# Kernel tuning notes

Measured on AMD Instinct MI355X. Metric: run time of the kernel, lower is better.

## Reference

```python
import jax, jax.numpy as jnp
import numpy as np

N_NODES = 1024
FEAT = 64
NEG_BIG = -9e15

def setup_inputs() -> dict:
    key = jax.random.key(0)
    ks = jax.random.split(key, 12)
    B, S, D = 4, 16384, FEAT
    flow_features = jax.random.normal(ks[0], (B, S, D), dtype=jnp.float32)
    src_ips = jax.random.randint(ks[1], (B, S), 0, N_NODES)
    dst_ips = jax.random.randint(ks[2], (B, S), 0, N_NODES)
    flow_volumes = jax.random.uniform(ks[3], (B, S), dtype=jnp.float32) * 2000.0
    emb = jax.random.normal(ks[4], (N_NODES, D), dtype=jnp.float32) * 0.02
    We1 = jax.random.normal(ks[5], (2 * D, 32), dtype=jnp.float32) * 0.1
    be1 = jnp.zeros((32,), dtype=jnp.float32)
    We2 = jax.random.normal(ks[6], (32, 1), dtype=jnp.float32) * 0.1
    be2 = jnp.zeros((1,), dtype=jnp.float32)
    W = jax.random.normal(ks[7], (D, D), dtype=jnp.float32) * 0.1
    a1 = jax.random.normal(ks[8], (D,), dtype=jnp.float32) * 0.1
    a2 = jax.random.normal(ks[9], (D,), dtype=jnp.float32) * 0.1
    return dict(flow_features=flow_features, src_ips=src_ips, dst_ips=dst_ips,
                flow_volumes=flow_volumes, emb=emb, We1=We1, be1=be1, We2=We2,
                be2=be2, W=W, a1=a1, a2=a2)

def _forward(flow_features, flow_volumes, emb, We1, be1, We2, be2, W, a1, a2,
             src_ips, dst_ips):
    B, S, D = flow_features.shape
    N = emb.shape[0]
    # --- DynamicGraphBuilder: scatter-add flow features at dst nodes ---
    node = jax.vmap(lambda f, d: jnp.zeros((N, D), f.dtype).at[d].add(f))(
        flow_features, dst_ips)                         # (B, N, D)
    nrm = jnp.maximum(jnp.linalg.norm(node, axis=-1, keepdims=True), 1e-12)
    h = node / nrm                                      # F.normalize(p=2)
    # --- edge weights: MLP over concat(src_emb, dst_emb), scaled by volume ---
    pair = jnp.concatenate([emb[src_ips], emb[dst_ips]], axis=-1)  # (B, S, 2D)
    mid = jax.nn.relu(pair @ We1 + be1)
    ew = jax.nn.sigmoid((mid @ We2 + be2)[..., 0])      # (B, S)
    w = ew * jax.nn.sigmoid(flow_volumes / 1000.0)
    adj = jax.vmap(lambda s, d, ww: jnp.zeros((N, N), ww.dtype)
                   .at[s, d].set(ww).at[d, s].set(ww))(src_ips, dst_ips, w)
    # --- GraphAttentionLayer (decomposed e_ij = a1.Wh_i + a2.Wh_j) ---
    Wh = h @ W                                          # (B, N, D)
    f1 = Wh @ a1                                        # (B, N)
    f2 = Wh @ a2                                        # (B, N)
    e = jax.nn.leaky_relu(f1[:, :, None] + f2[:, None, :], 0.2)  # (B, N, N)
    attn = jax.nn.softmax(jnp.where(adj > 0, e, NEG_BIG), axis=-1)
    return jax.nn.elu(jnp.einsum('bij,bjd->bid', attn, Wh))       # (B, N, D)

def reference(flow_features, src_ips, dst_ips, flow_volumes, emb, We1, be1,
              We2, be2, W, a1, a2):
    return _forward(flow_features, flow_volumes, emb, We1, be1, We2, be2,
                    W, a1, a2, src_ips, dst_ips)
```

## Files before the change

### kernel.cpp

```cpp
#include <hip/hip_runtime.h>
#include <math.h>

#define BB 4
#define SS 16384
#define NN 1024
#define DD 64
#define MW 32
#define CAP 256
#define JCAP 256

__device__ __forceinline__ float wave_sum(float v) {
    #pragma unroll
    for (int off = 32; off > 0; off >>= 1) v += __shfl_xor(v, off, 64);
    return v;
}
__device__ __forceinline__ float wave_max(float v) {
    #pragma unroll
    for (int off = 32; off > 0; off >>= 1) v = fmaxf(v, __shfl_xor(v, off, 64));
    return v;
}

__global__ __launch_bounds__(256) void build_kernel(
        const int* __restrict__ src_ips, const int* __restrict__ dst_ips,
        int* __restrict__ count, int* __restrict__ bucket,
        unsigned int* __restrict__ mask) {
    int tid = blockIdx.x * 256 + threadIdx.x;
    int b   = tid >> 14;
    int dst = dst_ips[tid];
    int src = src_ips[tid];
    int row = (b << 10) + dst;
    int pos = atomicAdd(count + row, 1);
    if (pos < CAP) bucket[row * CAP + pos] = tid;
    unsigned int* mb = mask + (size_t)b * NN * MW;
    atomicOr(mb + src * MW + (dst >> 5), 1u << (dst & 31));
    atomicOr(mb + dst * MW + (src >> 5), 1u << (src & 31));
}

__global__ __launch_bounds__(256) void gather_transform_kernel(
        const float* __restrict__ ff, const int* __restrict__ count,
        const int* __restrict__ bucket, const float* __restrict__ W,
        const float* __restrict__ a1, const float* __restrict__ a2,
        float* __restrict__ Wh, float* __restrict__ f1, float* __restrict__ f2) {
    __shared__ float Ws[DD * DD];
    __shared__ float hs[4][DD];
    __shared__ float a1s[DD], a2s[DD];
    int t = threadIdx.x;
    for (int i = t; i < DD * DD / 4; i += 256)
        ((float4*)Ws)[i] = ((const float4*)W)[i];
    if (t < DD) { a1s[t] = a1[t]; a2s[t] = a2[t]; }
    int wave = t >> 6, lane = t & 63;
    int fq = lane >> 4;
    int qi = lane & 15;
    int row = blockIdx.x * 4 + wave;

    int cnt = min(count[row], CAP);
    const int* bk = bucket + (size_t)row * CAP;
    int bkreg = (lane < cnt) ? bk[lane] : 0;
    float4 v = make_float4(0.f, 0.f, 0.f, 0.f);
    int lim = min(cnt, 64);
    for (int base = 0; base < lim; base += 4) {
        int fi = base + fq;
        int flow = __shfl(bkreg, fi, 64);
        if (fi < lim) {
            float4 x = ((const float4*)(ff + (size_t)flow * DD))[qi];
            v.x += x.x; v.y += x.y; v.z += x.z; v.w += x.w;
        }
    }
    for (int base = 64; base < cnt; base += 4) {
        int fi = base + fq;
        if (fi < cnt) {
            int flow = bk[fi];
            float4 x = ((const float4*)(ff + (size_t)flow * DD))[qi];
            v.x += x.x; v.y += x.y; v.z += x.z; v.w += x.w;
        }
    }
    #pragma unroll
    for (int off = 16; off <= 32; off <<= 1) {
        v.x += __shfl_xor(v.x, off, 64);
        v.y += __shfl_xor(v.y, off, 64);
        v.z += __shfl_xor(v.z, off, 64);
        v.w += __shfl_xor(v.w, off, 64);
    }
    float ssq = (fq == 0) ? (v.x*v.x + v.y*v.y + v.z*v.z + v.w*v.w) : 0.f;
    float nrm = fmaxf(sqrtf(wave_sum(ssq)), 1e-12f);
    float inv = 1.f / nrm;
    __syncthreads();
    if (fq == 0)
        ((float4*)hs[wave])[qi] = make_float4(v.x*inv, v.y*inv, v.z*inv, v.w*inv);
    float whl = 0.f;
    #pragma unroll
    for (int k = 0; k < DD; ++k)
        whl = fmaf(hs[wave][k], Ws[k * DD + lane], whl);
    Wh[row * DD + lane] = whl;
    float p1 = wave_sum(whl * a1s[lane]);
    float p2 = wave_sum(whl * a2s[lane]);
    if (lane == 0) { f1[row] = p1; f2[row] = p2; }
}

__global__ __launch_bounds__(256) void attn_kernel(
        const unsigned int* __restrict__ mask, const float* __restrict__ f1,
        const float* __restrict__ f2, const float* __restrict__ Wh,
        float* __restrict__ out) {
    __shared__ int   jls[4][JCAP];
    __shared__ float pls[4][JCAP];
    int t = threadIdx.x;
    int wave = t >> 6, lane = t & 63;
    int row = blockIdx.x * 4 + wave;
    int b = row >> 10;
    unsigned int mword = (lane < MW) ? mask[(size_t)row * MW + lane] : 0u;
    const float* f2b = f2 + b * NN;
    const float* Whb = Wh + (size_t)(b << 10) * DD;
    float f1i = f1[row];

    int pc = __popc(mword);
    int x = pc;
    #pragma unroll
    for (int off = 1; off < 64; off <<= 1) {
        int y = __shfl_up(x, off, 64);
        if (lane >= off) x += y;
    }
    int cnt = __shfl(x, 63, 64);
    int o = x - pc;
    if (cnt <= JCAP) {
        unsigned int bits = mword;
        while (bits) {
            int bidx = __ffs(bits) - 1; bits &= bits - 1;
            jls[wave][o++] = (lane << 5) + bidx;
        }
    }

    int fq = lane >> 4;
    int qi = lane & 15;

    if (cnt > 0 && cnt <= JCAP) {
        float m = -INFINITY;
        for (int k = lane; k < cnt; k += 64) {
            int j = jls[wave][k];
            float e = f1i + f2b[j];
            e = (e >= 0.f) ? e : 0.2f * e;
            m = fmaxf(m, e);
        }
        m = wave_max(m);
        float lsum = 0.f;
        for (int k = lane; k < cnt; k += 64) {
            int j = jls[wave][k];
            float e = f1i + f2b[j];
            e = (e >= 0.f) ? e : 0.2f * e;
            float p = __expf(e - m);
            pls[wave][k] = p;
            lsum += p;
        }
        lsum = wave_sum(lsum);
        float4 acc = make_float4(0.f, 0.f, 0.f, 0.f);
        for (int k = fq; k < cnt; k += 4) {
            int j   = jls[wave][k];
            float p = pls[wave][k];
            float4 w = ((const float4*)(Whb + (size_t)j * DD))[qi];
            acc.x = fmaf(p, w.x, acc.x);
            acc.y = fmaf(p, w.y, acc.y);
            acc.z = fmaf(p, w.z, acc.z);
            acc.w = fmaf(p, w.w, acc.w);
        }
        #pragma unroll
        for (int off = 16; off <= 32; off <<= 1) {
            acc.x += __shfl_xor(acc.x, off, 64);
            acc.y += __shfl_xor(acc.y, off, 64);
            acc.z += __shfl_xor(acc.z, off, 64);
            acc.w += __shfl_xor(acc.w, off, 64);
        }
        if (fq == 0) {
            float inv = 1.f / lsum;
            float4 r;
            r.x = acc.x * inv; r.y = acc.y * inv;
            r.z = acc.z * inv; r.w = acc.w * inv;
            r.x = (r.x > 0.f) ? r.x : expm1f(r.x);
            r.y = (r.y > 0.f) ? r.y : expm1f(r.y);
            r.z = (r.z > 0.f) ? r.z : expm1f(r.z);
            r.w = (r.w > 0.f) ? r.w : expm1f(r.w);
            ((float4*)(out + (size_t)row * DD))[qi] = r;
        }
    } else if (cnt == 0) {
        float4 acc = make_float4(0.f, 0.f, 0.f, 0.f);
        for (int k = fq; k < NN; k += 4) {
            float4 w = ((const float4*)(Whb + (size_t)k * DD))[qi];
            acc.x += w.x; acc.y += w.y; acc.z += w.z; acc.w += w.w;
        }
        #pragma unroll
        for (int off = 16; off <= 32; off <<= 1) {
            acc.x += __shfl_xor(acc.x, off, 64);
            acc.y += __shfl_xor(acc.y, off, 64);
            acc.z += __shfl_xor(acc.z, off, 64);
            acc.w += __shfl_xor(acc.w, off, 64);
        }
        if (fq == 0) {
            float4 r;
            r.x = acc.x * (1.f / NN); r.y = acc.y * (1.f / NN);
            r.z = acc.z * (1.f / NN); r.w = acc.w * (1.f / NN);
            r.x = (r.x > 0.f) ? r.x : expm1f(r.x);
            r.y = (r.y > 0.f) ? r.y : expm1f(r.y);
            r.z = (r.z > 0.f) ? r.z : expm1f(r.z);
            r.w = (r.w > 0.f) ? r.w : expm1f(r.w);
            ((float4*)(out + (size_t)row * DD))[qi] = r;
        }
    } else {
        float m = -INFINITY;
        for (int tt = 0; tt < 16; ++tt) {
            int j = lane + (tt << 6);
            unsigned int wv = __shfl(mword, j >> 5, 64);
            if (wv & (1u << (j & 31))) {
                float e = f1i + f2b[j];
                e = (e >= 0.f) ? e : 0.2f * e;
                m = fmaxf(m, e);
            }
        }
        m = wave_max(m);
        float lsum = 0.f;
        for (int tt = 0; tt < 16; ++tt) {
            int j = lane + (tt << 6);
            unsigned int wv = __shfl(mword, j >> 5, 64);
            if (wv & (1u << (j & 31))) {
                float e = f1i + f2b[j];
                e = (e >= 0.f) ? e : 0.2f * e;
                lsum += __expf(e - m);
            }
        }
        lsum = wave_sum(lsum);
        float acc = 0.f;
        for (int w = 0; w < MW; ++w) {
            unsigned int bits = __shfl(mword, w, 64);
            while (bits) {
                int j = (w << 5) + (__ffs(bits) - 1);
                bits &= bits - 1;
                float e = f1i + f2b[j];
                e = (e >= 0.f) ? e : 0.2f * e;
                acc = fmaf(__expf(e - m), Whb[(size_t)j * DD + lane], acc);
            }
        }
        acc /= lsum;
        out[(size_t)row * DD + lane] = (acc > 0.f) ? acc : expm1f(acc);
    }
}

extern "C" void kernel_launch(void* const* d_in, const int* in_sizes, int n_in,
                              void* d_out, int out_size, void* d_ws, size_t ws_size,
                              hipStream_t stream) {
    const float* ff      = (const float*)d_in[0];
    const int*   src_ips = (const int*)d_in[1];
    const int*   dst_ips = (const int*)d_in[2];
    const float* W  = (const float*)d_in[9];
    const float* a1 = (const float*)d_in[10];
    const float* a2 = (const float*)d_in[11];
    float* out = (float*)d_out;

    char* ws = (char*)d_ws;
    int* count         = (int*)ws;
    unsigned int* mask = (unsigned int*)(ws + (16 << 10));
    float* f1          = (float*)(ws + (528 << 10));
    float* f2          = (float*)(ws + (544 << 10));
    int* bucket        = (int*)(ws + (1 << 20));
    float* Wh          = (float*)(ws + (5 << 20));

    hipMemsetAsync(count, 0, (528 << 10), stream);

    build_kernel<<<BB * SS / 256, 256, 0, stream>>>(src_ips, dst_ips, count, bucket, mask);
    gather_transform_kernel<<<BB * NN / 4, 256, 0, stream>>>(ff, count, bucket, W, a1, a2, Wh, f1, f2);
    attn_kernel<<<BB * NN / 4, 256, 0, stream>>>(mask, f1, f2, Wh, out);
}
```

Baseline: 108.2 us.

## Replace global adjacency bitmask with per-node src/dst buckets built in shared memory

The build kernel no longer sets a 512KB global bitmask with atomicOr. It now records dst-side buckets, with the src node packed into the high bits, and src-side buckets holding the dst node. The attention kernel rebuilds each row's neighbor bitmask in shared memory from these two buckets, which also shrinks the memset. JCAP is raised so the dense fallback path can be dropped, and both the gather loop and the attention aggregation loop get two-way accumulator unrolling for more memory-level parallelism. The cost is a second bucket array and the extra per-row bucket reads in the attention kernel.

Result: faster. 103.6 us (-4.2%).

```diff
diff --git a/kernel.cpp b/kernel.cpp
--- a/kernel.cpp
+++ b/kernel.cpp
@@ -7,7 +7,7 @@
 #define DD 64
 #define MW 32
 #define CAP 256
-#define JCAP 256
+#define JCAP 512
 
 __device__ __forceinline__ float wave_sum(float v) {
     #pragma unroll
@@ -22,23 +22,23 @@
 
 __global__ __launch_bounds__(256) void build_kernel(
         const int* __restrict__ src_ips, const int* __restrict__ dst_ips,
-        int* __restrict__ count, int* __restrict__ bucket,
-        unsigned int* __restrict__ mask) {
+        int* __restrict__ cntd, int* __restrict__ cnts,
+        int* __restrict__ bucket_d, int* __restrict__ bucket_s) {
     int tid = blockIdx.x * 256 + threadIdx.x;
     int b   = tid >> 14;
     int dst = dst_ips[tid];
     int src = src_ips[tid];
-    int row = (b << 10) + dst;
-    int pos = atomicAdd(count + row, 1);
-    if (pos < CAP) bucket[row * CAP + pos] = tid;
-    unsigned int* mb = mask + (size_t)b * NN * MW;
-    atomicOr(mb + src * MW + (dst >> 5), 1u << (dst & 31));
-    atomicOr(mb + dst * MW + (src >> 5), 1u << (src & 31));
+    int rd = (b << 10) + dst;
+    int rs = (b << 10) + src;
+    int pd = atomicAdd(cntd + rd, 1);
+    if (pd < CAP) bucket_d[rd * CAP + pd] = tid | (src << 16);
+    int ps = atomicAdd(cnts + rs, 1);
+    if (ps < CAP) bucket_s[rs * CAP + ps] = dst;
 }
 
 __global__ __launch_bounds__(256) void gather_transform_kernel(
-        const float* __restrict__ ff, const int* __restrict__ count,
-        const int* __restrict__ bucket, const float* __restrict__ W,
+        const float* __restrict__ ff, const int* __restrict__ cntd,
+        const int* __restrict__ bucket_d, const float* __restrict__ W,
         const float* __restrict__ a1, const float* __restrict__ a2,
         float* __restrict__ Wh, float* __restrict__ f1, float* __restrict__ f2) {
     __shared__ float Ws[DD * DD];
@@ -53,27 +53,35 @@
     int qi = lane & 15;
     int row = blockIdx.x * 4 + wave;
 
-    int cnt = min(count[row], CAP);
-    const int* bk = bucket + (size_t)row * CAP;
+    int cnt = min(cntd[row], CAP);
+    const int* bk = bucket_d + (size_t)row * CAP;
     int bkreg = (lane < cnt) ? bk[lane] : 0;
-    float4 v = make_float4(0.f, 0.f, 0.f, 0.f);
+    float4 v0 = make_float4(0.f, 0.f, 0.f, 0.f);
+    float4 v1 = make_float4(0.f, 0.f, 0.f, 0.f);
     int lim = min(cnt, 64);
-    for (int base = 0; base < lim; base += 4) {
-        int fi = base + fq;
-        int flow = __shfl(bkreg, fi, 64);
-        if (fi < lim) {
-            float4 x = ((const float4*)(ff + (size_t)flow * DD))[qi];
-            v.x += x.x; v.y += x.y; v.z += x.z; v.w += x.w;
+    for (int base = 0; base < lim; base += 8) {
+        int fi0 = base + fq;
+        int fi1 = base + 4 + fq;
+        int w0 = __shfl(bkreg, fi0, 64);
+        int w1 = __shfl(bkreg, fi1, 64);
+        if (fi0 < lim) {
+            float4 x = ((const float4*)(ff + (size_t)(w0 & 0xFFFF) * DD))[qi];
+            v0.x += x.x; v0.y += x.y; v0.z += x.z; v0.w += x.w;
+        }
+        if (fi1 < lim) {
+            float4 x = ((const float4*)(ff + (size_t)(w1 & 0xFFFF) * DD))[qi];
+            v1.x += x.x; v1.y += x.y; v1.z += x.z; v1.w += x.w;
         }
     }
     for (int base = 64; base < cnt; base += 4) {
         int fi = base + fq;
         if (fi < cnt) {
-            int flow = bk[fi];
+            int flow = bk[fi] & 0xFFFF;
             float4 x = ((const float4*)(ff + (size_t)flow * DD))[qi];
-            v.x += x.x; v.y += x.y; v.z += x.z; v.w += x.w;
-        }
-    }
+            v0.x += x.x; v0.y += x.y; v0.z += x.z; v0.w += x.w;
+        }
+    }
+    float4 v = make_float4(v0.x + v1.x, v0.y + v1.y, v0.z + v1.z, v0.w + v1.w);
     #pragma unroll
     for (int off = 16; off <= 32; off <<= 1) {
         v.x += __shfl_xor(v.x, off, 64);
@@ -98,16 +106,31 @@
 }
 
 __global__ __launch_bounds__(256) void attn_kernel(
-        const unsigned int* __restrict__ mask, const float* __restrict__ f1,
-        const float* __restrict__ f2, const float* __restrict__ Wh,
-        float* __restrict__ out) {
+        const int* __restrict__ cntd, const int* __restrict__ cnts,
+        const int* __restrict__ bucket_d, const int* __restrict__ bucket_s,
+        const float* __restrict__ f1, const float* __restrict__ f2,
+        const float* __restrict__ Wh, float* __restrict__ out) {
+    __shared__ unsigned int bms[4][MW];
     __shared__ int   jls[4][JCAP];
     __shared__ float pls[4][JCAP];
     int t = threadIdx.x;
     int wave = t >> 6, lane = t & 63;
     int row = blockIdx.x * 4 + wave;
     int b = row >> 10;
-    unsigned int mword = (lane < MW) ? mask[(size_t)row * MW + lane] : 0u;
+    if (lane < MW) bms[wave][lane] = 0u;
+    int c1 = min(cntd[row], CAP);
+    int c2 = min(cnts[row], CAP);
+    const int* bd = bucket_d + (size_t)row * CAP;
+    const int* bs = bucket_s + (size_t)row * CAP;
+    for (int k = lane; k < c1; k += 64) {
+        int cand = (bd[k] >> 16) & 0x3FF;
+        atomicOr(&bms[wave][cand >> 5], 1u << (cand & 31));
+    }
+    for (int k = lane; k < c2; k += 64) {
+        int cand = bs[k] & 0x3FF;
+        atomicOr(&bms[wave][cand >> 5], 1u << (cand & 31));
+    }
+    unsigned int mword = (lane < MW) ? bms[wave][lane] : 0u;
     const float* f2b = f2 + b * NN;
     const float* Whb = Wh + (size_t)(b << 10) * DD;
     float f1i = f1[row];
@@ -121,7 +144,7 @@
     }
     int cnt = __shfl(x, 63, 64);
     int o = x - pc;
-    if (cnt <= JCAP) {
+    {
         unsigned int bits = mword;
         while (bits) {
             int bidx = __ffs(bits) - 1; bits &= bits - 1;
@@ -132,7 +155,7 @@
     int fq = lane >> 4;
     int qi = lane & 15;
 
-    if (cnt > 0 && cnt <= JCAP) {
+    if (cnt > 0) {
         float m = -INFINITY;
         for (int k = lane; k < cnt; k += 64) {
             int j = jls[wave][k];
@@ -151,16 +174,29 @@
             lsum += p;
         }
         lsum = wave_sum(lsum);
-        float4 acc = make_float4(0.f, 0.f, 0.f, 0.f);
-        for (int k = fq; k < cnt; k += 4) {
-            int j   = jls[wave][k];
-            float p = pls[wave][k];
-            float4 w = ((const float4*)(Whb + (size_t)j * DD))[qi];
-            acc.x = fmaf(p, w.x, acc.x);
-            acc.y = fmaf(p, w.y, acc.y);
-            acc.z = fmaf(p, w.z, acc.z);
-            acc.w = fmaf(p, w.w, acc.w);
-        }
+        float4 a0 = make_float4(0.f, 0.f, 0.f, 0.f);
+        float4 a1 = make_float4(0.f, 0.f, 0.f, 0.f);
+        for (int k = fq; k < cnt; k += 8) {
+            int j0   = jls[wave][k];
+            float p0 = pls[wave][k];
+            float4 w0 = ((const float4*)(Whb + (size_t)j0 * DD))[qi];
+            a0.x = fmaf(p0, w0.x, a0.x);
+            a0.y = fmaf(p0, w0.y, a0.y);
+            a0.z = fmaf(p0, w0.z, a0.z);
+            a0.w = fmaf(p0, w0.w, a0.w);
+            int k1 = k + 4;
+            if (k1 < cnt) {
+                int j1   = jls[wave][k1];
+                float p1 = pls[wave][k1];
+                float4 w1 = ((const float4*)(Whb + (size_t)j1 * DD))[qi];
+                a1.x = fmaf(p1, w1.x, a1.x);
+                a1.y = fmaf(p1, w1.y, a1.y);
+                a1.z = fmaf(p1, w1.z, a1.z);
+                a1.w = fmaf(p1, w1.w, a1.w);
+            }
+        }
+        float4 acc = make_float4(a0.x + a1.x, a0.y + a1.y,
+                                 a0.z + a1.z, a0.w + a1.w);
         #pragma unroll
         for (int off = 16; off <= 32; off <<= 1) {
             acc.x += __shfl_xor(acc.x, off, 64);
@@ -179,7 +215,7 @@
             r.w = (r.w > 0.f) ? r.w : expm1f(r.w);
             ((float4*)(out + (size_t)row * DD))[qi] = r;
         }
-    } else if (cnt == 0) {
+    } else {
         float4 acc = make_float4(0.f, 0.f, 0.f, 0.f);
         for (int k = fq; k < NN; k += 4) {
             float4 w = ((const float4*)(Whb + (size_t)k * DD))[qi];
@@ -202,42 +238,6 @@
             r.w = (r.w > 0.f) ? r.w : expm1f(r.w);
             ((float4*)(out + (size_t)row * DD))[qi] = r;
         }
-    } else {
-        float m = -INFINITY;
-        for (int tt = 0; tt < 16; ++tt) {
-            int j = lane + (tt << 6);
-            unsigned int wv = __shfl(mword, j >> 5, 64);
-            if (wv & (1u << (j & 31))) {
-                float e = f1i + f2b[j];
-                e = (e >= 0.f) ? e : 0.2f * e;
-                m = fmaxf(m, e);
-            }
-        }
-        m = wave_max(m);
-        float lsum = 0.f;
-        for (int tt = 0; tt < 16; ++tt) {
-            int j = lane + (tt << 6);
-            unsigned int wv = __shfl(mword, j >> 5, 64);
-            if (wv & (1u << (j & 31))) {
-                float e = f1i + f2b[j];
-                e = (e >= 0.f) ? e : 0.2f * e;
-                lsum += __expf(e - m);
-            }
-        }
-        lsum = wave_sum(lsum);
-        float acc = 0.f;
-        for (int w = 0; w < MW; ++w) {
-            unsigned int bits = __shfl(mword, w, 64);
-            while (bits) {
-                int j = (w << 5) + (__ffs(bits) - 1);
-                bits &= bits - 1;
-                float e = f1i + f2b[j];
-                e = (e >= 0.f) ? e : 0.2f * e;
-                acc = fmaf(__expf(e - m), Whb[(size_t)j * DD + lane], acc);
-            }
-        }
-        acc /= lsum;
-        out[(size_t)row * DD + lane] = (acc > 0.f) ? acc : expm1f(acc);
     }
 }
 
@@ -253,16 +253,20 @@
     float* out = (float*)d_out;
 
     char* ws = (char*)d_ws;
-    int* count         = (int*)ws;
-    unsigned int* mask = (unsigned int*)(ws + (16 << 10));
-    float* f1          = (float*)(ws + (528 << 10));
-    float* f2          = (float*)(ws + (544 << 10));
-    int* bucket        = (int*)(ws + (1 << 20));
-    float* Wh          = (float*)(ws + (5 << 20));
-
-    hipMemsetAsync(count, 0, (528 << 10), stream);
-
-    build_kernel<<<BB * SS / 256, 256, 0, stream>>>(src_ips, dst_ips, count, bucket, mask);
-    gather_transform_kernel<<<BB * NN / 4, 256, 0, stream>>>(ff, count, bucket, W, a1, a2, Wh, f1, f2);
-    attn_kernel<<<BB * NN / 4, 256, 0, stream>>>(mask, f1, f2, Wh, out);
-}
+    int* cntd       = (int*)ws;
+    int* cnts       = (int*)(ws + (16 << 10));
+    float* f1       = (float*)(ws + (32 << 10));
+    float* f2       = (float*)(ws + (48 << 10));
+    int* bucket_d   = (int*)(ws + (1 << 20));
+    int* bucket_s   = (int*)(ws + (5 << 20));
+    float* Wh       = (float*)(ws + (9 << 20));
+
+    hipMemsetAsync(cntd, 0, (32 << 10), stream);
+
+    build_kernel<<<BB * SS / 256, 256, 0, stream>>>(src_ips, dst_ips,
+                                                    cntd, cnts, bucket_d, bucket_s);
+    gather_transform_kernel<<<BB * NN / 4, 256, 0, stream>>>(ff, cntd, bucket_d,
+                                                             W, a1, a2, Wh, f1, f2);
+    attn_kernel<<<BB * NN / 4, 256, 0, stream>>>(cntd, cnts, bucket_d, bucket_s,
+                                                 f1, f2, Wh, out);
+}
```

## Replace global-atomic graph build with per-block index scans in shared memory

Applied to the files above, without the earlier changes.

Removes the memset and the global-atomic build kernel. Each block now scans the batch's whole dst (and src) index arrays to build its own per-row flow lists and adjacency bitmasks in shared memory, and each block handles 8 rows instead of 4. This trades global atomics, the extra launch and the bucket/mask global traffic for redundant reading of the index arrays: each block reads 64KB to 128KB of indices, with 512 blocks per kernel. The gather and accumulate loops are also unrolled by two. The per-row flow list is capped at 192 entries, and rows past that cap are silently truncated.

Result: slower. 110.7 us (+2.3%).

```diff
diff --git a/kernel.cpp b/kernel.cpp
--- a/kernel.cpp
+++ b/kernel.cpp
@@ -6,7 +6,8 @@
 #define NN 1024
 #define DD 64
 #define MW 32
-#define CAP 256
+#define RPB 8
+#define FCAP 192
 #define JCAP 256
 
 __device__ __forceinline__ float wave_sum(float v) {
@@ -20,224 +21,264 @@
     return v;
 }
 
-__global__ __launch_bounds__(256) void build_kernel(
-        const int* __restrict__ src_ips, const int* __restrict__ dst_ips,
-        int* __restrict__ count, int* __restrict__ bucket,
-        unsigned int* __restrict__ mask) {
-    int tid = blockIdx.x * 256 + threadIdx.x;
-    int b   = tid >> 14;
-    int dst = dst_ips[tid];
-    int src = src_ips[tid];
-    int row = (b << 10) + dst;
-    int pos = atomicAdd(count + row, 1);
-    if (pos < CAP) bucket[row * CAP + pos] = tid;
-    unsigned int* mb = mask + (size_t)b * NN * MW;
-    atomicOr(mb + src * MW + (dst >> 5), 1u << (dst & 31));
-    atomicOr(mb + dst * MW + (src >> 5), 1u << (src & 31));
-}
-
-__global__ __launch_bounds__(256) void gather_transform_kernel(
-        const float* __restrict__ ff, const int* __restrict__ count,
-        const int* __restrict__ bucket, const float* __restrict__ W,
-        const float* __restrict__ a1, const float* __restrict__ a2,
-        float* __restrict__ Wh, float* __restrict__ f1, float* __restrict__ f2) {
+__global__ __launch_bounds__(256) void gather_transform_scan(
+        const float* __restrict__ ff, const int* __restrict__ dst_ips,
+        const float* __restrict__ W, const float* __restrict__ a1,
+        const float* __restrict__ a2, float* __restrict__ Wh,
+        float* __restrict__ f1, float* __restrict__ f2) {
     __shared__ float Ws[DD * DD];
+    __shared__ float a1s[DD], a2s[DD];
     __shared__ float hs[4][DD];
-    __shared__ float a1s[DD], a2s[DD];
+    __shared__ int lcnt[RPB];
+    __shared__ int lst[RPB][FCAP];
     int t = threadIdx.x;
     for (int i = t; i < DD * DD / 4; i += 256)
         ((float4*)Ws)[i] = ((const float4*)W)[i];
     if (t < DD) { a1s[t] = a1[t]; a2s[t] = a2[t]; }
+    if (t < RPB) lcnt[t] = 0;
+    __syncthreads();
+
+    int blk = blockIdx.x;
+    int b = blk >> 7;
+    int n0 = (blk & 127) * RPB;
+    const int* db = dst_ips + b * SS;
+
+    for (int f4 = t; f4 < SS / 4; f4 += 256) {
+        int4 d = ((const int4*)db)[f4];
+        int f = f4 << 2;
+        #define CHK(c, off) { unsigned r = (unsigned)(c - n0); \
+            if (r < RPB) { int p = atomicAdd(&lcnt[r], 1); \
+                           if (p < FCAP) lst[r][p] = f + off; } }
+        CHK(d.x, 0) CHK(d.y, 1) CHK(d.z, 2) CHK(d.w, 3)
+        #undef CHK
+    }
+    __syncthreads();
+
     int wave = t >> 6, lane = t & 63;
     int fq = lane >> 4;
     int qi = lane & 15;
-    int row = blockIdx.x * 4 + wave;
-
-    int cnt = min(count[row], CAP);
-    const int* bk = bucket + (size_t)row * CAP;
-    int bkreg = (lane < cnt) ? bk[lane] : 0;
-    float4 v = make_float4(0.f, 0.f, 0.f, 0.f);
-    int lim = min(cnt, 64);
-    for (int base = 0; base < lim; base += 4) {
-        int fi = base + fq;
-        int flow = __shfl(bkreg, fi, 64);
-        if (fi < lim) {
-            float4 x = ((const float4*)(ff + (size_t)flow * DD))[qi];
-            v.x += x.x; v.y += x.y; v.z += x.z; v.w += x.w;
-        }
+    const float* ffb = ff + (size_t)b * SS * DD;
+
+    for (int rr = 0; rr < 2; ++rr) {
+        int lr = wave * 2 + rr;
+        int row = blk * RPB + lr;
+        int cnt = min(lcnt[lr], FCAP);
+        float4 v0 = make_float4(0.f, 0.f, 0.f, 0.f);
+        float4 v1 = make_float4(0.f, 0.f, 0.f, 0.f);
+        for (int k = fq; k < cnt; k += 8) {
+            int F0 = lst[lr][k];
+            float4 x = ((const float4*)(ffb + (size_t)F0 * DD))[qi];
+            v0.x += x.x; v0.y += x.y; v0.z += x.z; v0.w += x.w;
+            int k1 = k + 4;
+            if (k1 < cnt) {
+                int F1 = lst[lr][k1];
+                float4 y = ((const float4*)(ffb + (size_t)F1 * DD))[qi];
+                v1.x += y.x; v1.y += y.y; v1.z += y.z; v1.w += y.w;
+            }
+        }
+        float4 v = make_float4(v0.x + v1.x, v0.y + v1.y,
+                               v0.z + v1.z, v0.w + v1.w);
+        #pragma unroll
+        for (int off = 16; off <= 32; off <<= 1) {
+            v.x += __shfl_xor(v.x, off, 64);
+            v.y += __shfl_xor(v.y, off, 64);
+            v.z += __shfl_xor(v.z, off, 64);
+            v.w += __shfl_xor(v.w, off, 64);
+        }
+        float ssq = (fq == 0) ? (v.x*v.x + v.y*v.y + v.z*v.z + v.w*v.w) : 0.f;
+        float nrm = fmaxf(sqrtf(wave_sum(ssq)), 1e-12f);
+        float inv = 1.f / nrm;
+        if (fq == 0)
+            ((float4*)hs[wave])[qi] =
+                make_float4(v.x*inv, v.y*inv, v.z*inv, v.w*inv);
+        float whl = 0.f;
+        #pragma unroll
+        for (int k = 0; k < DD; ++k)
+            whl = fmaf(hs[wave][k], Ws[k * DD + lane], whl);
+        Wh[(size_t)row * DD + lane] = whl;
+        float p1 = wave_sum(whl * a1s[lane]);
+        float p2 = wave_sum(whl * a2s[lane]);
+        if (lane == 0) { f1[row] = p1; f2[row] = p2; }
     }
-    for (int base = 64; base < cnt; base += 4) {
-        int fi = base + fq;
-        if (fi < cnt) {
-            int flow = bk[fi];
-            float4 x = ((const float4*)(ff + (size_t)flow * DD))[qi];
-            v.x += x.x; v.y += x.y; v.z += x.z; v.w += x.w;
-        }
+}
+
+__global__ __launch_bounds__(256) void attn_scan(
+        const int* __restrict__ src_ips, const int* __restrict__ dst_ips,
+        const float* __restrict__ f1, const float* __restrict__ f2,
+        const float* __restrict__ Wh, float* __restrict__ out) {
+    __shared__ unsigned int bms[RPB][MW];
+    __shared__ int   jls[RPB][JCAP];
+    __shared__ float pls[RPB][JCAP];
+    int t = threadIdx.x;
+    bms[t >> 5][t & 31] = 0u;
+    __syncthreads();
+
+    int blk = blockIdx.x;
+    int b = blk >> 7;
+    int n0 = (blk & 127) * RPB;
+    const int* db = dst_ips + b * SS;
+    const int* sb = src_ips + b * SS;
+
+    for (int f4 = t; f4 < SS / 4; f4 += 256) {
+        int4 d = ((const int4*)db)[f4];
+        int4 s = ((const int4*)sb)[f4];
+        #define CHK(dc, sc) { \
+            unsigned r1 = (unsigned)(dc - n0); \
+            if (r1 < RPB) atomicOr(&bms[r1][sc >> 5], 1u << (sc & 31)); \
+            unsigned r2 = (unsigned)(sc - n0); \
+            if (r2 < RPB) atomicOr(&bms[r2][dc >> 5], 1u << (dc & 31)); }
+        CHK(d.x, s.x) CHK(d.y, s.y) CHK(d.z, s.z) CHK(d.w, s.w)
+        #undef CHK
     }
-    #pragma unroll
-    for (int off = 16; off <= 32; off <<= 1) {
-        v.x += __shfl_xor(v.x, off, 64);
-        v.y += __shfl_xor(v.y, off, 64);
-        v.z += __shfl_xor(v.z, off, 64);
-        v.w += __shfl_xor(v.w, off, 64);
-    }
-    float ssq = (fq == 0) ? (v.x*v.x + v.y*v.y + v.z*v.z + v.w*v.w) : 0.f;
-    float nrm = fmaxf(sqrtf(wave_sum(ssq)), 1e-12f);
-    float inv = 1.f / nrm;
     __syncthreads();
-    if (fq == 0)
-        ((float4*)hs[wave])[qi] = make_float4(v.x*inv, v.y*inv, v.z*inv, v.w*inv);
-    float whl = 0.f;
-    #pragma unroll
-    for (int k = 0; k < DD; ++k)
-        whl = fmaf(hs[wave][k], Ws[k * DD + lane], whl);
-    Wh[row * DD + lane] = whl;
-    float p1 = wave_sum(whl * a1s[lane]);
-    float p2 = wave_sum(whl * a2s[lane]);
-    if (lane == 0) { f1[row] = p1; f2[row] = p2; }
-}
-
-__global__ __launch_bounds__(256) void attn_kernel(
-        const unsigned int* __restrict__ mask, const float* __restrict__ f1,
-        const float* __restrict__ f2, const float* __restrict__ Wh,
-        float* __restrict__ out) {
-    __shared__ int   jls[4][JCAP];
-    __shared__ float pls[4][JCAP];
-    int t = threadIdx.x;
+
     int wave = t >> 6, lane = t & 63;
-    int row = blockIdx.x * 4 + wave;
-    int b = row >> 10;
-    unsigned int mword = (lane < MW) ? mask[(size_t)row * MW + lane] : 0u;
+    int fq = lane >> 4;
+    int qi = lane & 15;
     const float* f2b = f2 + b * NN;
     const float* Whb = Wh + (size_t)(b << 10) * DD;
-    float f1i = f1[row];
-
-    int pc = __popc(mword);
-    int x = pc;
-    #pragma unroll
-    for (int off = 1; off < 64; off <<= 1) {
-        int y = __shfl_up(x, off, 64);
-        if (lane >= off) x += y;
-    }
-    int cnt = __shfl(x, 63, 64);
-    int o = x - pc;
-    if (cnt <= JCAP) {
-        unsigned int bits = mword;
-        while (bits) {
-            int bidx = __ffs(bits) - 1; bits &= bits - 1;
-            jls[wave][o++] = (lane << 5) + bidx;
-        }
-    }
-
-    int fq = lane >> 4;
-    int qi = lane & 15;
-
-    if (cnt > 0 && cnt <= JCAP) {
-        float m = -INFINITY;
-        for (int k = lane; k < cnt; k += 64) {
-            int j = jls[wave][k];
-            float e = f1i + f2b[j];
-            e = (e >= 0.f) ? e : 0.2f * e;
-            m = fmaxf(m, e);
-        }
-        m = wave_max(m);
-        float lsum = 0.f;
-        for (int k = lane; k < cnt; k += 64) {
-            int j = jls[wave][k];
-            float e = f1i + f2b[j];
-            e = (e >= 0.f) ? e : 0.2f * e;
-            float p = __expf(e - m);
-            pls[wave][k] = p;
-            lsum += p;
-        }
-        lsum = wave_sum(lsum);
-        float4 acc = make_float4(0.f, 0.f, 0.f, 0.f);
-        for (int k = fq; k < cnt; k += 4) {
-            int j   = jls[wave][k];
-            float p = pls[wave][k];
-            float4 w = ((const float4*)(Whb + (size_t)j * DD))[qi];
-            acc.x = fmaf(p, w.x, acc.x);
-            acc.y = fmaf(p, w.y, acc.y);
-            acc.z = fmaf(p, w.z, acc.z);
-            acc.w = fmaf(p, w.w, acc.w);
-        }
+
+    for (int rr = 0; rr < 2; ++rr) {
+        int lr = wave * 2 + rr;
+        int row = blk * RPB + lr;
+        float f1i = f1[row];
+        unsigned int mword = (lane < MW) ? bms[lr][lane] : 0u;
+
+        int pc = __popc(mword);
+        int x = pc;
         #pragma unroll
-        for (int off = 16; off <= 32; off <<= 1) {
-            acc.x += __shfl_xor(acc.x, off, 64);
-            acc.y += __shfl_xor(acc.y, off, 64);
-            acc.z += __shfl_xor(acc.z, off, 64);
-            acc.w += __shfl_xor(acc.w, off, 64);
-        }
-        if (fq == 0) {
-            float inv = 1.f / lsum;
-            float4 r;
-            r.x = acc.x * inv; r.y = acc.y * inv;
-            r.z = acc.z * inv; r.w = acc.w * inv;
-            r.x = (r.x > 0.f) ? r.x : expm1f(r.x);
-            r.y = (r.y > 0.f) ? r.y : expm1f(r.y);
-            r.z = (r.z > 0.f) ? r.z : expm1f(r.z);
-            r.w = (r.w > 0.f) ? r.w : expm1f(r.w);
-            ((float4*)(out + (size_t)row * DD))[qi] = r;
-        }
-    } else if (cnt == 0) {
-        float4 acc = make_float4(0.f, 0.f, 0.f, 0.f);
-        for (int k = fq; k < NN; k += 4) {
-            float4 w = ((const float4*)(Whb + (size_t)k * DD))[qi];
-            acc.x += w.x; acc.y += w.y; acc.z += w.z; acc.w += w.w;
-        }
-        #pragma unroll
-        for (int off = 16; off <= 32; off <<= 1) {
-            acc.x += __shfl_xor(acc.x, off, 64);
-            acc.y += __shfl_xor(acc.y, off, 64);
-            acc.z += __shfl_xor(acc.z, off, 64);
-            acc.w += __shfl_xor(acc.w, off, 64);
-        }
-        if (fq == 0) {
-            float4 r;
-            r.x = acc.x * (1.f / NN); r.y = acc.y * (1.f / NN);
-            r.z = acc.z * (1.f / NN); r.w = acc.w * (1.f / NN);
-            r.x = (r.x > 0.f) ? r.x : expm1f(r.x);
-            r.y = (r.y > 0.f) ? r.y : expm1f(r.y);
-            r.z = (r.z > 0.f) ? r.z : expm1f(r.z);
-            r.w = (r.w > 0.f) ? r.w : expm1f(r.w);
-            ((float4*)(out + (size_t)row * DD))[qi] = r;
-        }
-    } else {
-        float m = -INFINITY;
-        for (int tt = 0; tt < 16; ++tt) {
-            int j = lane + (tt << 6);
-            unsigned int wv = __shfl(mword, j >> 5, 64);
-            if (wv & (1u << (j & 31))) {
+        for (int off = 1; off < 64; off <<= 1) {
+            int y = __shfl_up(x, off, 64);
+            if (lane >= off) x += y;
+        }
+        int cnt = __shfl(x, 63, 64);
+        int o = x - pc;
+        if (cnt <= JCAP) {
+            unsigned int bits = mword;
+            while (bits) {
+                int bidx = __ffs(bits) - 1; bits &= bits - 1;
+                jls[lr][o++] = (lane << 5) + bidx;
+            }
+        }
+
+        if (cnt > 0 && cnt <= JCAP) {
+            float m = -INFINITY;
+            for (int k = lane; k < cnt; k += 64) {
+                int j = jls[lr][k];
                 float e = f1i + f2b[j];
                 e = (e >= 0.f) ? e : 0.2f * e;
                 m = fmaxf(m, e);
             }
-        }
-        m = wave_max(m);
-        float lsum = 0.f;
-        for (int tt = 0; tt < 16; ++tt) {
-            int j = lane + (tt << 6);
-            unsigned int wv = __shfl(mword, j >> 5, 64);
-            if (wv & (1u << (j & 31))) {
+            m = wave_max(m);
+            float lsum = 0.f;
+            for (int k = lane; k < cnt; k += 64) {
+                int j = jls[lr][k];
                 float e = f1i + f2b[j];
                 e = (e >= 0.f) ? e : 0.2f * e;
-                lsum += __expf(e - m);
-            }
-        }
-        lsum = wave_sum(lsum);
-        float acc = 0.f;
-        for (int w = 0; w < MW; ++w) {
-            unsigned int bits = __shfl(mword, w, 64);
-            while (bits) {
-                int j = (w << 5) + (__ffs(bits) - 1);
-                bits &= bits - 1;
-                float e = f1i + f2b[j];
-                e = (e >= 0.f) ? e : 0.2f * e;
-                acc = fmaf(__expf(e - m), Whb[(size_t)j * DD + lane], acc);
-            }
-        }
-        acc /= lsum;
-        out[(size_t)row * DD + lane] = (acc > 0.f) ? acc : expm1f(acc);
+                float p = __expf(e - m);
+                pls[lr][k] = p;
+                lsum += p;
+            }
+            lsum = wave_sum(lsum);
+            float4 a0 = make_float4(0.f, 0.f, 0.f, 0.f);
+            float4 a1v = make_float4(0.f, 0.f, 0.f, 0.f);
+            for (int k = fq; k < cnt; k += 8) {
+                int j0   = jls[lr][k];
+                float p0 = pls[lr][k];
+                float4 w0 = ((const float4*)(Whb + (size_t)j0 * DD))[qi];
+                a0.x = fmaf(p0, w0.x, a0.x);
+                a0.y = fmaf(p0, w0.y, a0.y);
+                a0.z = fmaf(p0, w0.z, a0.z);
+                a0.w = fmaf(p0, w0.w, a0.w);
+                int k1 = k + 4;
+                if (k1 < cnt) {
+                    int j1   = jls[lr][k1];
+                    float p1 = pls[lr][k1];
+                    float4 w1 = ((const float4*)(Whb + (size_t)j1 * DD))[qi];
+                    a1v.x = fmaf(p1, w1.x, a1v.x);
+                    a1v.y = fmaf(p1, w1.y, a1v.y);
+                    a1v.z = fmaf(p1, w1.z, a1v.z);
+                    a1v.w = fmaf(p1, w1.w, a1v.w);
+                }
+            }
+            float4 acc = make_float4(a0.x + a1v.x, a0.y + a1v.y,
+                                     a0.z + a1v.z, a0.w + a1v.w);
+            #pragma unroll
+            for (int off = 16; off <= 32; off <<= 1) {
+                acc.x += __shfl_xor(acc.x, off, 64);
+                acc.y += __shfl_xor(acc.y, off, 64);
+                acc.z += __shfl_xor(acc.z, off, 64);
+                acc.w += __shfl_xor(acc.w, off, 64);
+            }
+            if (fq == 0) {
+                float inv = 1.f / lsum;
+                float4 r;
+                r.x = acc.x * inv; r.y = acc.y * inv;
+                r.z = acc.z * inv; r.w = acc.w * inv;
+                r.x = (r.x > 0.f) ? r.x : expm1f(r.x);
+                r.y = (r.y > 0.f) ? r.y : expm1f(r.y);
+                r.z = (r.z > 0.f) ? r.z : expm1f(r.z);
+                r.w = (r.w > 0.f) ? r.w : expm1f(r.w);
+                ((float4*)(out + (size_t)row * DD))[qi] = r;
+            }
+        } else if (cnt == 0) {
+            float4 acc = make_float4(0.f, 0.f, 0.f, 0.f);
+            for (int k = fq; k < NN; k += 4) {
+                float4 w = ((const float4*)(Whb + (size_t)k * DD))[qi];
+                acc.x += w.x; acc.y += w.y; acc.z += w.z; acc.w += w.w;
+            }
+            #pragma unroll
+            for (int off = 16; off <= 32; off <<= 1) {
+                acc.x += __shfl_xor(acc.x, off, 64);
+                acc.y += __shfl_xor(acc.y, off, 64);
+                acc.z += __shfl_xor(acc.z, off, 64);
+                acc.w += __shfl_xor(acc.w, off, 64);
+            }
+            if (fq == 0) {
+                float4 r;
+                r.x = acc.x * (1.f / NN); r.y = acc.y * (1.f / NN);
+                r.z = acc.z * (1.f / NN); r.w = acc.w * (1.f / NN);
+                r.x = (r.x > 0.f) ? r.x : expm1f(r.x);
+                r.y = (r.y > 0.f) ? r.y : expm1f(r.y);
+                r.z = (r.z > 0.f) ? r.z : expm1f(r.z);
+                r.w = (r.w > 0.f) ? r.w : expm1f(r.w);
+                ((float4*)(out + (size_t)row * DD))[qi] = r;
+            }
+        } else {
+            float m = -INFINITY;
+            for (int tt = 0; tt < 16; ++tt) {
+                int j = lane + (tt << 6);
+                if (bms[lr][j >> 5] & (1u << (j & 31))) {
+                    float e = f1i + f2b[j];
+                    e = (e >= 0.f) ? e : 0.2f * e;
+                    m = fmaxf(m, e);
+                }
+            }
+            m = wave_max(m);
+            float lsum = 0.f;
+            for (int tt = 0; tt < 16; ++tt) {
+                int j = lane + (tt << 6);
+                if (bms[lr][j >> 5] & (1u << (j & 31))) {
+                    float e = f1i + f2b[j];
+                    e = (e >= 0.f) ? e : 0.2f * e;
+                    lsum += __expf(e - m);
+                }
+            }
+            lsum = wave_sum(lsum);
+            float acc = 0.f;
+            for (int w = 0; w < MW; ++w) {
+                unsigned int bits = bms[lr][w];
+                while (bits) {
+                    int j = (w << 5) + (__ffs(bits) - 1);
+                    bits &= bits - 1;
+                    float e = f1i + f2b[j];
+                    e = (e >= 0.f) ? e : 0.2f * e;
+                    acc = fmaf(__expf(e - m), Whb[(size_t)j * DD + lane], acc);
+                }
+            }
+            acc /= lsum;
+            out[(size_t)row * DD + lane] = (acc > 0.f) ? acc : expm1f(acc);
+        }
     }
 }
 
@@ -253,16 +294,12 @@
     float* out = (float*)d_out;
 
     char* ws = (char*)d_ws;
-    int* count         = (int*)ws;
-    unsigned int* mask = (unsigned int*)(ws + (16 << 10));
-    float* f1          = (float*)(ws + (528 << 10));
-    float* f2          = (float*)(ws + (544 << 10));
-    int* bucket        = (int*)(ws + (1 << 20));
-    float* Wh          = (float*)(ws + (5 << 20));
-
-    hipMemsetAsync(count, 0, (528 << 10), stream);
-
-    build_kernel<<<BB * SS / 256, 256, 0, stream>>>(src_ips, dst_ips, count, bucket, mask);
-    gather_transform_kernel<<<BB * NN / 4, 256, 0, stream>>>(ff, count, bucket, W, a1, a2, Wh, f1, f2);
-    attn_kernel<<<BB * NN / 4, 256, 0, stream>>>(mask, f1, f2, Wh, out);
-}
+    float* Wh = (float*)ws;
+    float* f1 = (float*)(ws + (1 << 20));
+    float* f2 = (float*)(ws + (1 << 20) + (16 << 10));
+
+    gather_transform_scan<<<BB * NN / RPB, 256, 0, stream>>>(
+        ff, dst_ips, W, a1, a2, Wh, f1, f2);
+    attn_scan<<<BB * NN / RPB, 256, 0, stream>>>(
+        src_ips, dst_ips, f1, f2, Wh, out);
+}
```
